# Optimization experiments

Measured on AMD Instinct MI355X. Metric: run time of the kernel, lower is better.

Reference implementation:

```python
import jax, jax.numpy as jnp
import numpy as np

B, T, NEMBD, NVOCAB, HID = 32, 64, 64, 256, 4096


def setup_inputs() -> dict:
    key = jax.random.key(0)
    ks = jax.random.split(key, 12)
    s = 0.1  # keep activations in a sane range
    return {
        "X": jax.random.randint(ks[0], (B, T), 0, NVOCAB, dtype=jnp.int32),
        "M": jnp.ones((B, T, 1), dtype=jnp.float32),
        "S": jnp.zeros((2, B, HID), dtype=jnp.float32),
        "embd": jax.random.normal(ks[1], (NVOCAB, NEMBD), jnp.float32) * s,
        "wx": jax.random.normal(ks[2], (NEMBD, 4 * HID), jnp.float32) * s,
        "wh": jax.random.normal(ks[3], (HID, 4 * HID), jnp.float32) * s,
        "wmx": jax.random.normal(ks[4], (NEMBD, HID), jnp.float32) * s,
        "wmh": jax.random.normal(ks[5], (HID, HID), jnp.float32) * s,
        "b": jnp.zeros((4 * HID,), jnp.float32),
        "gx": jax.random.normal(ks[6], (4 * HID,), jnp.float32),
        "gh": jax.random.normal(ks[7], (4 * HID,), jnp.float32),
        "gmx": jax.random.normal(ks[8], (HID,), jnp.float32),
        "gmh": jax.random.normal(ks[9], (HID,), jnp.float32),
        "w_out": jax.random.normal(ks[10], (HID, NVOCAB), jnp.float32) * s,
        "b_out": jnp.zeros((NVOCAB,), jnp.float32),
    }


def _wn(w, g):
    # tf.nn.l2_normalize(w, dim=0) * g  (column-wise weight norm)
    return w * (g / jnp.sqrt(jnp.sum(w * w, axis=0, keepdims=True).clip(1e-12)))


def reference(X, M, S, embd, wx, wh, wmx, wmh, b, gx, gh, gmx, gmh, w_out, b_out):
    # weight-normalized rnn weights (rnn_wn=True)
    wxn, whn = _wn(wx, gx), _wn(wh, gh)
    wmxn, wmhn = _wn(wmx, gmx), _wn(wmh, gmh)

    words = embd[X]                       # [B,T,64]
    xs = jnp.swapaxes(words, 0, 1)        # [T,B,64]
    ms = jnp.swapaxes(M, 0, 1)            # [T,B,1]
    c0, h0 = S[0], S[1]                   # [B,HID] each

    def step(carry, inp):
        c, h = carry
        x, mt = inp
        m = (x @ wmxn) * (h @ wmhn)       # multiplicative intermediate
        z = x @ wxn + m @ whn + b         # [B,4*HID]
        i, f, o, u = jnp.split(z, 4, axis=1)
        i, f, o = jax.nn.sigmoid(i), jax.nn.sigmoid(f), jax.nn.sigmoid(o)
        u = jnp.tanh(u)
        ct = f * c + i * u
        ht = o * jnp.tanh(ct)
        c = ct * mt + c * (1.0 - mt)      # mask-blend state
        h = ht * mt + h * (1.0 - mt)
        return (c, h), (c, h)

    (cf, hf), (cells, hs) = jax.lax.scan(step, (c0, h0), (xs, ms))
    states = jnp.stack([cf, hf], 0)       # [2,B,HID]
    # tf.concat(hs,1) then reshape [-1,HID] => batch-major (b, t) row order
    hflat = jnp.swapaxes(hs, 0, 1).reshape(-1, hs.shape[-1])  # [B*T,HID]
    logits = hflat @ w_out + b_out        # out_wn=False
    return cells, states, logits
```

## Files before the change

### kernel.cpp

```cpp
#include <hip/hip_runtime.h>
#include <hip/hip_bf16.h>

#define HID 4096
#define NEMBD 64
#define NBATCH 32
#define NTIME 64
#define NVOCAB 256
#define G4 16384

typedef __attribute__((ext_vector_type(4))) float f32x4;
typedef __attribute__((ext_vector_type(8))) short s16x8;

__device__ __forceinline__ unsigned short f2bf(float f) {
  union { float f; unsigned u; } v; v.f = f;
  unsigned u = v.u + 0x7FFFu + ((v.u >> 16) & 1u);
  return (unsigned short)(u >> 16);
}

__device__ __forceinline__ int apoff(int b, int j) {
  return ((j >> 5) << 10) | ((b >> 4) << 9) |
         (((b & 15) | (((j >> 3) & 3) << 4)) << 3) | (j & 7);
}

__global__ void colsum_k(const float* __restrict__ w, float* __restrict__ ss,
                         int K, int N, int KS) {
  int col = threadIdx.x & 63, kg = threadIdx.x >> 6;
  int j = blockIdx.x * 64 + col;
  int kper = K / KS;
  int k0 = blockIdx.y * kper;
  float s = 0.f;
#pragma unroll 4
  for (int k = k0 + kg; k < k0 + kper; k += 4) {
    float v = w[(size_t)k * N + j];
    s += v * v;
  }
  __shared__ float red[4][64];
  red[kg][col] = s;
  __syncthreads();
  if (threadIdx.x < 64)
    ss[(size_t)blockIdx.y * N + j] = red[0][col] + red[1][col] + red[2][col] + red[3][col];
}

__global__ void pack_k(const float* __restrict__ src, const float* __restrict__ ss,
                       const float* __restrict__ g, unsigned short* __restrict__ dst,
                       int N, int Cw, int S, int nch, int KS) {
  int bid = blockIdx.x;
  int colbase = (bid & 3) * Cw + (bid >> S) * 16;
  int cper = nch / gridDim.y;
  int c0 = blockIdx.y * cper;
  size_t dstbase = (size_t)bid * nch * 512 + (size_t)c0 * 512;
  __shared__ unsigned short tile[512];
  int tid = threadIdx.x;
  int col16 = tid & 15, kk = tid >> 4;
  float sc = 1.f;
  if (ss) {
    float t = 0.f;
    for (int q = 0; q < KS; ++q) t += ss[(size_t)q * N + colbase + col16];
    sc = g[colbase + col16] / sqrtf(fmaxf(t, 1e-12f));
  }
  for (int c = c0; c < c0 + cper; ++c) {
    for (int h = 0; h < 2; ++h) {
      int kk2 = kk + h * 16;
      int k = c * 32 + kk2;
      float v = src[(size_t)k * N + colbase + col16] * sc;
      int l = col16 | (((kk2 >> 3) & 3) << 4);
      tile[l * 8 + (kk2 & 7)] = f2bf(v);
    }
    __syncthreads();
    if (tid < 64)
      ((s16x8*)(dst + dstbase + (size_t)(c - c0) * 512))[tid] = ((s16x8*)tile)[tid];
    __syncthreads();
  }
}

__global__ void xepack_k(const int* __restrict__ X, const float* __restrict__ embd,
                         unsigned short* __restrict__ xe) {
  int t = blockIdx.x;
  int tid = threadIdx.x;
  int l = tid & 63, tile = (tid >> 6) & 1, c2 = tid >> 7;
  int b = tile * 16 + (l & 15);
  int row = X[b * NTIME + t];
  int k0 = 32 * c2 + 8 * (l >> 4);
  size_t off = (size_t)t * 2048 + c2 * 1024 + tile * 512 + l * 8;
  for (int j = 0; j < 8; ++j) xe[off + j] = f2bf(embd[row * NEMBD + k0 + j]);
}

__global__ void init_k(const float* __restrict__ S, float* __restrict__ cst,
                       float* __restrict__ hst, unsigned short* __restrict__ hpk) {
  int e = blockIdx.x * 256 + threadIdx.x;
  if (e < NBATCH * HID) {
    float c = S[e], h = S[NBATCH * HID + e];
    cst[e] = c; hst[e] = h;
    int b = e >> 12, j = e & 4095;
    hpk[apoff(b, j)] = f2bf(h);
  }
}

#define MFMA(a, b, c) __builtin_amdgcn_mfma_f32_16x16x32_bf16(a, b, c, 0, 0, 0)

__global__ __launch_bounds__(1024, 4)
void ph1_k(const unsigned short* __restrict__ wmhp, const unsigned short* __restrict__ wmxp,
           const unsigned short* __restrict__ xe, const unsigned short* __restrict__ hpk,
           unsigned short* __restrict__ mpk, int t) {
  const int g = blockIdx.x;
  const int tid = threadIdx.x;
  const int w = tid >> 6, l = tid & 63;
  const int lo = l & 15, hi = l >> 4;

  __shared__ float part[16][32][16];
  __shared__ float xmS[32][16];

  const s16x8* wmh_g = (const s16x8*)(wmhp + (size_t)g * 128 * 512);
  const s16x8* wmx_g = (const s16x8*)(wmxp + (size_t)g * 2 * 512);
  const s16x8* hp = (const s16x8*)hpk;

  f32x4 a0 = {0.f, 0.f, 0.f, 0.f}, a1 = {0.f, 0.f, 0.f, 0.f};
  const int cb = w * 8;
  {
    s16x8 wbuf[4], pa[4], pb[4];
#pragma unroll
    for (int q = 0; q < 4; ++q) {
      wbuf[q] = wmh_g[(cb + q) * 64 + l];
      pa[q] = hp[(cb + q) * 128 + l];
      pb[q] = hp[(cb + q) * 128 + 64 + l];
    }
#pragma unroll
    for (int q = 0; q < 8; ++q) {
      const int r = q & 3;
      s16x8 bf = wbuf[r], af = pa[r], gf = pb[r];
      if (q < 4) {
        wbuf[r] = wmh_g[(cb + q + 4) * 64 + l];
        pa[r] = hp[(cb + q + 4) * 128 + l];
        pb[r] = hp[(cb + q + 4) * 128 + 64 + l];
      }
      a0 = MFMA(af, bf, a0);
      a1 = MFMA(gf, bf, a1);
    }
  }
#pragma unroll
  for (int r = 0; r < 4; ++r) {
    part[w][4 * hi + r][lo] = a0[r];
    part[w][16 + 4 * hi + r][lo] = a1[r];
  }
  if (w == 0) {
    f32x4 x0 = {0.f, 0.f, 0.f, 0.f}, x1 = {0.f, 0.f, 0.f, 0.f};
    const s16x8* xep = (const s16x8*)(xe + (size_t)t * 2048);
#pragma unroll
    for (int c2 = 0; c2 < 2; ++c2) {
      s16x8 bf = wmx_g[c2 * 64 + l];
      x0 = MFMA(xep[c2 * 128 + l], bf, x0);
      x1 = MFMA(xep[c2 * 128 + 64 + l], bf, x1);
    }
#pragma unroll
    for (int r = 0; r < 4; ++r) {
      xmS[4 * hi + r][lo] = x0[r];
      xmS[16 + 4 * hi + r][lo] = x1[r];
    }
  }
  __syncthreads();
  if (tid < 512) {
    const int eb = tid >> 4, c = tid & 15;
    const int ej = g * 16 + c;
    float hm = 0.f;
#pragma unroll
    for (int k = 0; k < 16; ++k) hm += part[k][eb][c];
    mpk[apoff(eb, ej)] = f2bf(xmS[eb][c] * hm);
  }
}

__global__ __launch_bounds__(1024, 4)
void ph2_k(const unsigned short* __restrict__ whp, const unsigned short* __restrict__ wxp,
           const unsigned short* __restrict__ xe, const float* __restrict__ bias,
           const float* __restrict__ Mm, const unsigned short* __restrict__ mpk,
           unsigned short* __restrict__ hpk, float* __restrict__ cst,
           float* __restrict__ hst, unsigned short* __restrict__ hflat,
           float* __restrict__ out, int t) {
  const int g = blockIdx.x;
  const int tid = threadIdx.x;
  const int w = tid >> 6, l = tid & 63;
  const int lo = l & 15, hi = l >> 4;
  const int gate = w & 3, ks = w >> 2;

  __shared__ float part[16][32][16];

  const s16x8* wh_w = (const s16x8*)(whp + (size_t)(g * 4 + gate) * 128 * 512);
  const s16x8* wx_w = (const s16x8*)(wxp + (size_t)(g * 4 + gate) * 2 * 512);
  const s16x8* mp = (const s16x8*)mpk;

  f32x4 z0 = {0.f, 0.f, 0.f, 0.f}, z1 = {0.f, 0.f, 0.f, 0.f};
  const int cb = ks * 32;
  {
    s16x8 wbuf[4], pa[4], pb[4];
#pragma unroll
    for (int q = 0; q < 4; ++q) {
      wbuf[q] = wh_w[(cb + q) * 64 + l];
      pa[q] = mp[(cb + q) * 128 + l];
      pb[q] = mp[(cb + q) * 128 + 64 + l];
    }
#pragma unroll
    for (int q = 0; q < 32; ++q) {
      const int r = q & 3;
      s16x8 bf = wbuf[r], af = pa[r], gf = pb[r];
      if (q < 28) {
        wbuf[r] = wh_w[(cb + q + 4) * 64 + l];
        pa[r] = mp[(cb + q + 4) * 128 + l];
        pb[r] = mp[(cb + q + 4) * 128 + 64 + l];
      }
      z0 = MFMA(af, bf, z0);
      z1 = MFMA(gf, bf, z1);
    }
  }
  if (ks == 0) {
    const s16x8* xep = (const s16x8*)(xe + (size_t)t * 2048);
#pragma unroll
    for (int c2 = 0; c2 < 2; ++c2) {
      s16x8 bf = wx_w[c2 * 64 + l];
      z0 = MFMA(xep[c2 * 128 + l], bf, z0);
      z1 = MFMA(xep[c2 * 128 + 64 + l], bf, z1);
    }
  }
#pragma unroll
  for (int r = 0; r < 4; ++r) {
    part[w][4 * hi + r][lo] = z0[r];
    part[w][16 + 4 * hi + r][lo] = z1[r];
  }
  __syncthreads();
  if (tid < 512) {
    const int eb = tid >> 4, c = tid & 15;
    const int ej = g * 16 + c;
    float iv = part[0][eb][c] + part[4][eb][c] + part[8][eb][c] + part[12][eb][c] + bias[ej];
    float fv = part[1][eb][c] + part[5][eb][c] + part[9][eb][c] + part[13][eb][c] + bias[4096 + ej];
    float ov = part[2][eb][c] + part[6][eb][c] + part[10][eb][c] + part[14][eb][c] + bias[8192 + ej];
    float uv = part[3][eb][c] + part[7][eb][c] + part[11][eb][c] + part[15][eb][c] + bias[12288 + ej];
    iv = 1.f / (1.f + __expf(-iv));
    fv = 1.f / (1.f + __expf(-fv));
    ov = 1.f / (1.f + __expf(-ov));
    uv = tanhf(uv);
    size_t sj = (size_t)eb * HID + ej;
    float cp = cst[sj], hpv = hst[sj];
    float ct = fv * cp + iv * uv;
    float ht = ov * tanhf(ct);
    float mt = Mm[eb * NTIME + t];
    float cn = ct * mt + cp * (1.f - mt);
    float hn = ht * mt + hpv * (1.f - mt);
    cst[sj] = cn;
    hst[sj] = hn;
    out[((size_t)t * NBATCH + eb) * HID + ej] = cn;
    unsigned short hb = f2bf(hn);
    {
      int tle = eb * 4 + (t >> 4);
      int r16 = t & 15;
      int kk2 = ej & 31;
      int lane2 = r16 | (((kk2 >> 3) & 3) << 4);
      hflat[(size_t)tle * 65536 + (size_t)(ej >> 5) * 512 + lane2 * 8 + (kk2 & 7)] = hb;
    }
    hpk[apoff(eb, ej)] = hb;
    if (t == NTIME - 1) {
      out[(size_t)NTIME * NBATCH * HID + sj] = cn;
      out[(size_t)NTIME * NBATCH * HID + NBATCH * HID + sj] = hn;
    }
  }
}

__global__ __launch_bounds__(256)
void logits_k(const unsigned short* __restrict__ hpA,
              const unsigned short* __restrict__ woutp,
              const float* __restrict__ bout, float* __restrict__ out) {
  int tle = blockIdx.x >> 1, ch = blockIdx.x & 1;
  int tid = threadIdx.x, w = tid >> 6, l = tid & 63;
  int lo = l & 15, hi = l >> 4;
  const s16x8* ap = (const s16x8*)(hpA + (size_t)tle * 65536);
  const s16x8* wp = (const s16x8*)woutp;
  f32x4 acc[2] = {{0.f,0.f,0.f,0.f},{0.f,0.f,0.f,0.f}};
  const int nt0 = ch * 8 + w * 2;
#pragma unroll 4
  for (int c = 0; c < 128; ++c) {
    s16x8 af = ap[c * 64 + l];
    acc[0] = MFMA(af, wp[((nt0 + 0) * 128 + c) * 64 + l], acc[0]);
    acc[1] = MFMA(af, wp[((nt0 + 1) * 128 + c) * 64 + l], acc[1]);
  }
  int r0 = tle * 16;
#pragma unroll
  for (int q = 0; q < 2; ++q) {
    int col = (nt0 + q) * 16 + lo;
    float bo = bout[col];
#pragma unroll
    for (int r = 0; r < 4; ++r)
      out[(size_t)(r0 + 4 * hi + r) * NVOCAB + col] = acc[q][r] + bo;
  }
}

extern "C" void kernel_launch(void* const* d_in, const int* in_sizes, int n_in,
                              void* d_out, int out_size, void* d_ws, size_t ws_size,
                              hipStream_t stream) {
  const int*   X    = (const int*)d_in[0];
  const float* Mm   = (const float*)d_in[1];
  const float* S    = (const float*)d_in[2];
  const float* embd = (const float*)d_in[3];
  const float* wx   = (const float*)d_in[4];
  const float* wh   = (const float*)d_in[5];
  const float* wmx  = (const float*)d_in[6];
  const float* wmh  = (const float*)d_in[7];
  const float* b    = (const float*)d_in[8];
  const float* gx   = (const float*)d_in[9];
  const float* gh   = (const float*)d_in[10];
  const float* gmx  = (const float*)d_in[11];
  const float* gmh  = (const float*)d_in[12];
  const float* wout = (const float*)d_in[13];
  const float* bout = (const float*)d_in[14];
  float* out = (float*)d_out;
  char* ws = (char*)d_ws;

  size_t cur = 0;
  auto alloc = [&](size_t bytes) { size_t o = cur; cur += (bytes + 255) & ~size_t(255); return o; };
  unsigned short* WHP   = (unsigned short*)(ws + alloc((size_t)1024 * 128 * 512 * 2));
  unsigned short* WMHP  = (unsigned short*)(ws + alloc((size_t)256 * 128 * 512 * 2));
  unsigned short* WXP   = (unsigned short*)(ws + alloc((size_t)1024 * 2 * 512 * 2));
  unsigned short* WMXP  = (unsigned short*)(ws + alloc((size_t)256 * 2 * 512 * 2));
  unsigned short* WOUTP = (unsigned short*)(ws + alloc((size_t)16 * 128 * 512 * 2));
  unsigned short* XE    = (unsigned short*)(ws + alloc((size_t)64 * 2048 * 2));
  unsigned short* MPK   = (unsigned short*)(ws + alloc((size_t)32 * 4096 * 2));
  unsigned short* HPK   = (unsigned short*)(ws + alloc((size_t)32 * 4096 * 2));
  float* CST            = (float*)(ws + alloc((size_t)32 * 4096 * 4));
  float* HST            = (float*)(ws + alloc((size_t)32 * 4096 * 4));
  unsigned short* HFLAT = (unsigned short*)(ws + alloc((size_t)2048 * 4096 * 2));
  float* SSH            = (float*)(ws + alloc((size_t)8 * 16384 * 4));
  float* SSMH           = (float*)(ws + alloc((size_t)8 * 4096 * 4));
  float* SSX            = (float*)(ws + alloc((size_t)16384 * 4));
  float* SSMX           = (float*)(ws + alloc((size_t)4096 * 4));
  (void)ws_size; (void)in_sizes; (void)n_in; (void)out_size;

  colsum_k<<<dim3(256, 8), 256, 0, stream>>>(wh,  SSH,  HID, G4,  8);
  colsum_k<<<dim3(64, 8),  256, 0, stream>>>(wmh, SSMH, HID, HID, 8);
  colsum_k<<<dim3(256, 1), 256, 0, stream>>>(wx,  SSX,  NEMBD, G4,  1);
  colsum_k<<<dim3(64, 1),  256, 0, stream>>>(wmx, SSMX, NEMBD, HID, 1);

  pack_k<<<dim3(1024, 8), 256, 0, stream>>>(wh,  SSH,  gh,  WHP,  G4,  4096, 2, 128, 8);
  pack_k<<<dim3(256, 4),  256, 0, stream>>>(wmh, SSMH, gmh, WMHP, HID, 0,    0, 128, 8);
  pack_k<<<dim3(1024, 1), 256, 0, stream>>>(wx,  SSX,  gx,  WXP,  G4,  4096, 2, 2,   1);
  pack_k<<<dim3(256, 1),  256, 0, stream>>>(wmx, SSMX, gmx, WMXP, HID, 0,    0, 2,   1);
  pack_k<<<dim3(16, 1),   256, 0, stream>>>(wout, nullptr, nullptr, WOUTP, NVOCAB, 0, 0, 128, 0);

  xepack_k<<<64, 256, 0, stream>>>(X, embd, XE);
  init_k<<<512, 256, 0, stream>>>(S, CST, HST, HPK);

  for (int t = 0; t < NTIME; ++t) {
    ph1_k<<<256, 1024, 0, stream>>>(WMHP, WMXP, XE, HPK, MPK, t);
    ph2_k<<<256, 1024, 0, stream>>>(WHP, WXP, XE, b, Mm, MPK, HPK, CST, HST, HFLAT, out, t);
  }

  logits_k<<<256, 256, 0, stream>>>(HFLAT, WOUTP, bout,
                                    out + (size_t)NTIME * NBATCH * HID + 2 * NBATCH * HID);
}
```

Baseline: 2.422 ms.

## Fuse weight-norm column sums into packing and apply scales in epilogues

Removes the separate column-sum-of-squares kernels and instead computes the norms while packing the raw weights to bf16, so each weight matrix is read once instead of twice. The per-column scale is no longer baked into packed weights; it is applied in the ph1/ph2 epilogues (splitting the x-path accumulator so its scale can differ). This shifts precision slightly (unscaled bf16 weights) and adds a few scale loads per timestep, and the pack grid loses its k-split parallelism.

```diff
diff --git a/kernel.cpp b/kernel.cpp
--- a/kernel.cpp
+++ b/kernel.cpp
@@ -22,54 +22,39 @@
          (((b & 15) | (((j >> 3) & 3) << 4)) << 3) | (j & 7);
 }
 
-__global__ void colsum_k(const float* __restrict__ w, float* __restrict__ ss,
-                         int K, int N, int KS) {
-  int col = threadIdx.x & 63, kg = threadIdx.x >> 6;
-  int j = blockIdx.x * 64 + col;
-  int kper = K / KS;
-  int k0 = blockIdx.y * kper;
-  float s = 0.f;
-#pragma unroll 4
-  for (int k = k0 + kg; k < k0 + kper; k += 4) {
-    float v = w[(size_t)k * N + j];
-    s += v * v;
-  }
-  __shared__ float red[4][64];
-  red[kg][col] = s;
-  __syncthreads();
-  if (threadIdx.x < 64)
-    ss[(size_t)blockIdx.y * N + j] = red[0][col] + red[1][col] + red[2][col] + red[3][col];
-}
-
-__global__ void pack_k(const float* __restrict__ src, const float* __restrict__ ss,
-                       const float* __restrict__ g, unsigned short* __restrict__ dst,
-                       int N, int Cw, int S, int nch, int KS) {
+__global__ void packs_k(const float* __restrict__ src, const float* __restrict__ g,
+                        unsigned short* __restrict__ dst, float* __restrict__ sc,
+                        int N, int Cw, int S, int nch) {
   int bid = blockIdx.x;
   int colbase = (bid & 3) * Cw + (bid >> S) * 16;
-  int cper = nch / gridDim.y;
-  int c0 = blockIdx.y * cper;
-  size_t dstbase = (size_t)bid * nch * 512 + (size_t)c0 * 512;
+  size_t dstbase = (size_t)bid * nch * 512;
   __shared__ unsigned short tile[512];
+  __shared__ float red[16][16];
   int tid = threadIdx.x;
   int col16 = tid & 15, kk = tid >> 4;
-  float sc = 1.f;
-  if (ss) {
-    float t = 0.f;
-    for (int q = 0; q < KS; ++q) t += ss[(size_t)q * N + colbase + col16];
-    sc = g[colbase + col16] / sqrtf(fmaxf(t, 1e-12f));
-  }
-  for (int c = c0; c < c0 + cper; ++c) {
-    for (int h = 0; h < 2; ++h) {
-      int kk2 = kk + h * 16;
-      int k = c * 32 + kk2;
-      float v = src[(size_t)k * N + colbase + col16] * sc;
-      int l = col16 | (((kk2 >> 3) & 3) << 4);
-      tile[l * 8 + (kk2 & 7)] = f2bf(v);
-    }
+  float s = 0.f;
+  for (int c = 0; c < nch; ++c) {
+    float v0 = src[(size_t)(c * 32 + kk) * N + colbase + col16];
+    float v1 = src[(size_t)(c * 32 + kk + 16) * N + colbase + col16];
+    s += v0 * v0 + v1 * v1;
+    int l0 = col16 | (((kk >> 3) & 3) << 4);
+    int l1 = col16 | ((((kk + 16) >> 3) & 3) << 4);
+    tile[l0 * 8 + (kk & 7)] = f2bf(v0);
+    tile[l1 * 8 + (kk & 7)] = f2bf(v1);
     __syncthreads();
     if (tid < 64)
-      ((s16x8*)(dst + dstbase + (size_t)(c - c0) * 512))[tid] = ((s16x8*)tile)[tid];
+      ((s16x8*)(dst + dstbase + (size_t)c * 512))[tid] = ((s16x8*)tile)[tid];
     __syncthreads();
+  }
+  if (g) {
+    red[kk][col16] = s;
+    __syncthreads();
+    if (tid < 16) {
+      float tot = 0.f;
+#pragma unroll
+      for (int q = 0; q < 16; ++q) tot += red[q][tid];
+      sc[colbase + tid] = g[colbase + tid] / sqrtf(fmaxf(tot, 1e-12f));
+    }
   }
 }
 
@@ -101,6 +86,7 @@
 __global__ __launch_bounds__(1024, 4)
 void ph1_k(const unsigned short* __restrict__ wmhp, const unsigned short* __restrict__ wmxp,
            const unsigned short* __restrict__ xe, const unsigned short* __restrict__ hpk,
+           const float* __restrict__ scmh, const float* __restrict__ scmx,
            unsigned short* __restrict__ mpk, int t) {
   const int g = blockIdx.x;
   const int tid = threadIdx.x;
@@ -164,13 +150,14 @@
     float hm = 0.f;
 #pragma unroll
     for (int k = 0; k < 16; ++k) hm += part[k][eb][c];
-    mpk[apoff(eb, ej)] = f2bf(xmS[eb][c] * hm);
+    mpk[apoff(eb, ej)] = f2bf(xmS[eb][c] * hm * (scmh[ej] * scmx[ej]));
   }
 }
 
 __global__ __launch_bounds__(1024, 4)
 void ph2_k(const unsigned short* __restrict__ whp, const unsigned short* __restrict__ wxp,
            const unsigned short* __restrict__ xe, const float* __restrict__ bias,
+           const float* __restrict__ sch, const float* __restrict__ scx,
            const float* __restrict__ Mm, const unsigned short* __restrict__ mpk,
            unsigned short* __restrict__ hpk, float* __restrict__ cst,
            float* __restrict__ hst, unsigned short* __restrict__ hflat,
@@ -182,6 +169,7 @@
   const int gate = w & 3, ks = w >> 2;
 
   __shared__ float part[16][32][16];
+  __shared__ float xpart[4][32][16];
 
   const s16x8* wh_w = (const s16x8*)(whp + (size_t)(g * 4 + gate) * 128 * 512);
   const s16x8* wx_w = (const s16x8*)(wxp + (size_t)(g * 4 + gate) * 2 * 512);
@@ -211,12 +199,18 @@
     }
   }
   if (ks == 0) {
+    f32x4 x0 = {0.f, 0.f, 0.f, 0.f}, x1 = {0.f, 0.f, 0.f, 0.f};
     const s16x8* xep = (const s16x8*)(xe + (size_t)t * 2048);
 #pragma unroll
     for (int c2 = 0; c2 < 2; ++c2) {
       s16x8 bf = wx_w[c2 * 64 + l];
-      z0 = MFMA(xep[c2 * 128 + l], bf, z0);
-      z1 = MFMA(xep[c2 * 128 + 64 + l], bf, z1);
+      x0 = MFMA(xep[c2 * 128 + l], bf, x0);
+      x1 = MFMA(xep[c2 * 128 + 64 + l], bf, x1);
+    }
+#pragma unroll
+    for (int r = 0; r < 4; ++r) {
+      xpart[gate][4 * hi + r][lo] = x0[r];
+      xpart[gate][16 + 4 * hi + r][lo] = x1[r];
     }
   }
 #pragma unroll
@@ -228,10 +222,15 @@
   if (tid < 512) {
     const int eb = tid >> 4, c = tid & 15;
     const int ej = g * 16 + c;
-    float iv = part[0][eb][c] + part[4][eb][c] + part[8][eb][c] + part[12][eb][c] + bias[ej];
-    float fv = part[1][eb][c] + part[5][eb][c] + part[9][eb][c] + part[13][eb][c] + bias[4096 + ej];
-    float ov = part[2][eb][c] + part[6][eb][c] + part[10][eb][c] + part[14][eb][c] + bias[8192 + ej];
-    float uv = part[3][eb][c] + part[7][eb][c] + part[11][eb][c] + part[15][eb][c] + bias[12288 + ej];
+    float zh, iv, fv, ov, uv;
+    zh = part[0][eb][c] + part[4][eb][c] + part[8][eb][c] + part[12][eb][c];
+    iv = zh * sch[ej] + xpart[0][eb][c] * scx[ej] + bias[ej];
+    zh = part[1][eb][c] + part[5][eb][c] + part[9][eb][c] + part[13][eb][c];
+    fv = zh * sch[4096 + ej] + xpart[1][eb][c] * scx[4096 + ej] + bias[4096 + ej];
+    zh = part[2][eb][c] + part[6][eb][c] + part[10][eb][c] + part[14][eb][c];
+    ov = zh * sch[8192 + ej] + xpart[2][eb][c] * scx[8192 + ej] + bias[8192 + ej];
+    zh = part[3][eb][c] + part[7][eb][c] + part[11][eb][c] + part[15][eb][c];
+    uv = zh * sch[12288 + ej] + xpart[3][eb][c] * scx[12288 + ej] + bias[12288 + ej];
     iv = 1.f / (1.f + __expf(-iv));
     fv = 1.f / (1.f + __expf(-fv));
     ov = 1.f / (1.f + __expf(-ov));
@@ -324,29 +323,25 @@
   float* CST            = (float*)(ws + alloc((size_t)32 * 4096 * 4));
   float* HST            = (float*)(ws + alloc((size_t)32 * 4096 * 4));
   unsigned short* HFLAT = (unsigned short*)(ws + alloc((size_t)2048 * 4096 * 2));
-  float* SSH            = (float*)(ws + alloc((size_t)8 * 16384 * 4));
-  float* SSMH           = (float*)(ws + alloc((size_t)8 * 4096 * 4));
-  float* SSX            = (float*)(ws + alloc((size_t)16384 * 4));
-  float* SSMX           = (float*)(ws + alloc((size_t)4096 * 4));
+  float* SCH            = (float*)(ws + alloc((size_t)16384 * 4));
+  float* SCX            = (float*)(ws + alloc((size_t)16384 * 4));
+  float* SCMH           = (float*)(ws + alloc((size_t)4096 * 4));
+  float* SCMX           = (float*)(ws + alloc((size_t)4096 * 4));
   (void)ws_size; (void)in_sizes; (void)n_in; (void)out_size;
 
-  colsum_k<<<dim3(256, 8), 256, 0, stream>>>(wh,  SSH,  HID, G4,  8);
-  colsum_k<<<dim3(64, 8),  256, 0, stream>>>(wmh, SSMH, HID, HID, 8);
-  colsum_k<<<dim3(256, 1), 256, 0, stream>>>(wx,  SSX,  NEMBD, G4,  1);
-  colsum_k<<<dim3(64, 1),  256, 0, stream>>>(wmx, SSMX, NEMBD, HID, 1);
-
-  pack_k<<<dim3(1024, 8), 256, 0, stream>>>(wh,  SSH,  gh,  WHP,  G4,  4096, 2, 128, 8);
-  pack_k<<<dim3(256, 4),  256, 0, stream>>>(wmh, SSMH, gmh, WMHP, HID, 0,    0, 128, 8);
-  pack_k<<<dim3(1024, 1), 256, 0, stream>>>(wx,  SSX,  gx,  WXP,  G4,  4096, 2, 2,   1);
-  pack_k<<<dim3(256, 1),  256, 0, stream>>>(wmx, SSMX, gmx, WMXP, HID, 0,    0, 2,   1);
-  pack_k<<<dim3(16, 1),   256, 0, stream>>>(wout, nullptr, nullptr, WOUTP, NVOCAB, 0, 0, 128, 0);
+  packs_k<<<1024, 256, 0, stream>>>(wh,   gh,  WHP,   SCH,  G4,    4096, 2, 128);
+  packs_k<<<256,  256, 0, stream>>>(wmh,  gmh, WMHP,  SCMH, HID,   0,    0, 128);
+  packs_k<<<1024, 256, 0, stream>>>(wx,   gx,  WXP,   SCX,  G4,    4096, 2, 2);
+  packs_k<<<256,  256, 0, stream>>>(wmx,  gmx, WMXP,  SCMX, HID,   0,    0, 2);
+  packs_k<<<16,   256, 0, stream>>>(wout, nullptr, WOUTP, nullptr, NVOCAB, 0, 0, 128);
 
   xepack_k<<<64, 256, 0, stream>>>(X, embd, XE);
   init_k<<<512, 256, 0, stream>>>(S, CST, HST, HPK);
 
   for (int t = 0; t < NTIME; ++t) {
-    ph1_k<<<256, 1024, 0, stream>>>(WMHP, WMXP, XE, HPK, MPK, t);
-    ph2_k<<<256, 1024, 0, stream>>>(WHP, WXP, XE, b, Mm, MPK, HPK, CST, HST, HFLAT, out, t);
+    ph1_k<<<256, 1024, 0, stream>>>(WMHP, WMXP, XE, HPK, SCMH, SCMX, MPK, t);
+    ph2_k<<<256, 1024, 0, stream>>>(WHP, WXP, XE, b, SCH, SCX, Mm, MPK, HPK, CST, HST,
+                                    HFLAT, out, t);
   }
 
   logits_k<<<256, 256, 0, stream>>>(HFLAT, WOUTP, bout,
```

Measured after the change: 2.414 ms, median of 2. About the same (-0.4%).
